# Kernel tuning notes

Hardware: AMD Instinct MI355X
Metric: run time of the kernel (lower is better)

## Reference

```python
import jax, jax.numpy as jnp
import numpy as np

BS, NUM_PATCH, N_VARS, PATCH_LEN, D_MODEL = 32, 64, 321, 12, 128
TIME_RATIO, FREQ_RATIO = 0.5, 0.4


def setup_inputs() -> dict:
    key = jax.random.key(0)
    ks = jax.random.split(key, 7)
    x = jax.random.normal(ks[0], (BS, NUM_PATCH, N_VARS, PATCH_LEN), jnp.float32)
    W_in = jax.random.normal(ks[1], (PATCH_LEN, D_MODEL), jnp.float32) / np.sqrt(PATCH_LEN)
    b_in = jnp.zeros((D_MODEL,), jnp.float32)
    W_out = jax.random.normal(ks[2], (D_MODEL, PATCH_LEN), jnp.float32) / np.sqrt(D_MODEL)
    b_out = jnp.zeros((PATCH_LEN,), jnp.float32)
    # nn.Parameter(torch.zeros(1,1,1)) in the original; use small random scalars so grads are non-trivial
    time_mask_token = jax.random.normal(ks[3], (), jnp.float32) * 0.02
    freq_mask_token = jax.random.normal(ks[4], (), jnp.float32) * 0.02
    return {"x": x, "W_in": W_in, "b_in": b_in, "W_out": W_out, "b_out": b_out,
            "time_mask_token": time_mask_token, "freq_mask_token": freq_mask_token}


def _scatter_mask(idx, num_patch):
    # idx: [bs, n_vars, k] patch indices to mask (set False). Returns bool [bs, num_patch, n_vars].
    bs, nv, k = idx.shape
    m = jnp.ones((bs, num_patch, nv), dtype=bool)
    b = jnp.arange(bs)[:, None, None]
    v = jnp.arange(nv)[None, :, None]
    return m.at[b, idx, v].set(False)


def reference(x, W_in, b_in, W_out, b_out, time_mask_token, freq_mask_token):
    bs, num_patch, n_vars, patch_len = x.shape

    # patch2emb applied per token (equivalent to the gather-encode path since the
    # projection is pointwise per patch): [bs, np, nv, d_model]
    emb = jnp.einsum('bpvl,ld->bpvd', x, W_in) + b_in

    # ---- time masking: mask patches with highest coefficient of variation ----
    cv = jnp.std(x, axis=-1, ddof=1) / (jnp.mean(x, axis=-1) + 1e-6)  # [bs, np, nv]
    k_t = int(num_patch * TIME_RATIO)
    _, idx_t = jax.lax.top_k(jnp.transpose(cv, (0, 2, 1)), k_t)       # [bs, nv, k_t]
    mask_t = _scatter_mask(idx_t, num_patch)                           # True = keep
    tokens_t = jnp.where(mask_t[..., None], emb, time_mask_token)
    out_t = jnp.einsum('bpvd,dl->bpvl', tokens_t, W_out) + b_out

    # ---- freq masking: mask patches with lowest mean FFT magnitude ----
    mag = jnp.abs(jnp.fft.rfft(x, axis=-1))                            # [bs, np, nv, pl//2+1]
    score = mag.mean(axis=-1)                                          # [bs, np, nv]
    k_f = int(num_patch * FREQ_RATIO)
    _, idx_f = jax.lax.top_k(-jnp.transpose(score, (0, 2, 1)), k_f)    # smallest scores
    mask_f = _scatter_mask(idx_f, num_patch)
    tokens_f = jnp.where(mask_f[..., None], emb, freq_mask_token)
    out_f = jnp.einsum('bpvd,dl->bpvl', tokens_f, W_out) + b_out

    return out_t * 0.5 + out_f * 0.5
```

## Files before the change

kernel.cpp:

```cpp
#include <hip/hip_runtime.h>
#include <math.h>

constexpr int BS = 32, NV = 321, PL = 12, DM = 128;
constexpr int KT = 32;
constexpr int KF = 25;
constexpr int VB = 8;
constexpr int NCHUNK = 41;
constexpr int SST = 72;

__device__ __forceinline__ unsigned ord(float f) {
  unsigned u = __float_as_uint(f);
  return ((int)u < 0) ? ~u : (u | 0x80000000u);
}

__global__ void prep_kernel(const float* __restrict__ W_in,
                            const float* __restrict__ b_in,
                            const float* __restrict__ W_out,
                            const float* __restrict__ b_out,
                            const float* __restrict__ tt,
                            const float* __restrict__ ft,
                            float* __restrict__ prep) {
  int t = threadIdx.x;
  if (t < 144) {
    int i = t / 12, l = t % 12;
    const float4* Wi = (const float4*)(W_in + i * DM);
    float s = 0.f;
#pragma unroll 8
    for (int d4 = 0; d4 < 32; ++d4) {
      float4 a = Wi[d4];
      const float* wo = W_out + d4 * 48 + l;
      s += a.x * wo[0] + a.y * wo[12] + a.z * wo[24] + a.w * wo[36];
    }
    prep[t] = s;
  } else if (t < 168) {
    int l = (t - 144) % 12;
    float cs = 0.f, cb = 0.f;
#pragma unroll 8
    for (int d = 0; d < DM; ++d) {
      float w = W_out[d * 12 + l];
      cs += w;
      cb += b_in[d] * w;
    }
    if (t < 156) {
      prep[144 + l] = cb;
      prep[156 + l] = tt[0] * cs;
    } else {
      prep[168 + l] = ft[0] * cs;
    }
  } else if (t < 180) {
    prep[180 + (t - 168)] = b_out[t - 168];
  }
}

__global__ __launch_bounds__(256) void fused_kernel(
    const float* __restrict__ x, const float* __restrict__ prep,
    float* __restrict__ out) {
  __shared__ float scv[VB * SST];
  __shared__ float sfs[VB * SST];
  __shared__ __align__(16) float spp[192];
  __shared__ unsigned long long smT[VB], smF[VB];

  const int t = threadIdx.x;
  const int chunk = blockIdx.x;
  const int b = blockIdx.y;
  const int v0 = chunk * VB;
  const bool full = (chunk < 40);
  const int nv = full ? VB : 1;

  const float* xb = x + ((size_t)(b * 64) * NV + v0) * PL;

  float xr[2][12];
  int pp[2], vvv[2];
  if (full) {
#pragma unroll
    for (int h = 0; h < 2; ++h) {
      const int j = t + 256 * h;
      const int p = j >> 3, vv = j & 7;
      pp[h] = p;
      vvv[h] = vv;
      const float4* src = (const float4*)(xb + ((size_t)p * NV + vv) * PL);
      float4 a = src[0], bb = src[1], c = src[2];
      xr[h][0] = a.x;  xr[h][1] = a.y;  xr[h][2] = a.z;  xr[h][3] = a.w;
      xr[h][4] = bb.x; xr[h][5] = bb.y; xr[h][6] = bb.z; xr[h][7] = bb.w;
      xr[h][8] = c.x;  xr[h][9] = c.y;  xr[h][10] = c.z; xr[h][11] = c.w;
    }
  } else {
    pp[0] = t & 63;
    vvv[0] = 0;
    pp[1] = 0;
    vvv[1] = 0;
    if (t < 64) {
      const float4* src = (const float4*)(xb + (size_t)t * NV * PL);
      float4 a = src[0], bb = src[1], c = src[2];
      xr[0][0] = a.x;  xr[0][1] = a.y;  xr[0][2] = a.z;  xr[0][3] = a.w;
      xr[0][4] = bb.x; xr[0][5] = bb.y; xr[0][6] = bb.z; xr[0][7] = bb.w;
      xr[0][8] = c.x;  xr[0][9] = c.y;  xr[0][10] = c.z; xr[0][11] = c.w;
    }
  }

  if (t < 192) spp[t] = prep[t];

  const float H = 0.86602540378443864676f;
#pragma unroll
  for (int h = 0; h < 2; ++h) {
    const bool valid = full || (h == 0 && t < 64);
    if (valid) {
      const float* xv = xr[h];
      float s = 0.f;
#pragma unroll
      for (int i = 0; i < 12; ++i) s += xv[i];
      const float m = s * (1.0f / 12.0f);
      float ss = 0.f;
#pragma unroll
      for (int i = 0; i < 12; ++i) {
        float d = xv[i] - m;
        ss += d * d;
      }
      const float cv = sqrtf(ss * (1.0f / 11.0f)) / (m + 1e-6f);

      const float e1 = xv[1] + xv[11], e2 = xv[2] + xv[10], e3 = xv[3] + xv[9],
                  e4 = xv[4] + xv[8], e5 = xv[5] + xv[7];
      const float o1 = xv[1] - xv[11], o2 = xv[2] - xv[10], o3 = xv[3] - xv[9],
                  o4 = xv[4] - xv[8], o5 = xv[5] - xv[7];
      float mag = fabsf(xv[0] + xv[6] + e1 + e2 + e3 + e4 + e5);
      float re = xv[0] - xv[6] + H * (e1 - e5) + 0.5f * (e2 - e4);
      float im = 0.5f * (o1 + o5) + H * (o2 + o4) + o3;
      mag += sqrtf(re * re + im * im);
      re = xv[0] + xv[6] + 0.5f * (e1 + e5) - 0.5f * (e2 + e4) - e3;
      im = H * (o1 + o2 - o4 - o5);
      mag += sqrtf(re * re + im * im);
      re = xv[0] - xv[6] - e2 + e4;
      im = o1 - o3 + o5;
      mag += sqrtf(re * re + im * im);
      re = xv[0] + xv[6] - 0.5f * (e1 + e2 + e4 + e5) + e3;
      im = H * (o1 - o2 + o4 - o5);
      mag += sqrtf(re * re + im * im);
      re = xv[0] - xv[6] + H * (e5 - e1) + 0.5f * (e2 - e4);
      im = 0.5f * (o1 + o5) - H * (o2 + o4) + o3;
      mag += sqrtf(re * re + im * im);
      re = xv[0] + xv[6] - e1 + e2 - e3 + e4 - e5;
      mag += fabsf(re);
      const float fs = mag * (1.0f / 7.0f);

      scv[vvv[h] * SST + pp[h]] = cv;
      sfs[vvv[h] * SST + pp[h]] = fs;
    }
  }
  __syncthreads();

  const int wv = t >> 6, lane = t & 63;
#pragma unroll
  for (int k = 0; k < 2; ++k) {
    const int vv = wv * 2 + k;
    if (vv < nv) {
      const unsigned ut = ord(scv[vv * SST + lane]);
      const unsigned uf = ~ord(sfs[vv * SST + lane]);
      unsigned tht = 0, thf = 0;
#pragma unroll
      for (int bit = 31; bit >= 0; --bit) {
        const unsigned ct = tht | (1u << bit);
        const unsigned cf = thf | (1u << bit);
        const unsigned long long bt = __ballot(ut >= ct);
        const unsigned long long bf = __ballot(uf >= cf);
        if (__popcll(bt) >= KT) tht = ct;
        if (__popcll(bf) >= KF) thf = cf;
      }
      const unsigned long long pre = (1ull << lane) - 1ull;
      const int gt_t = __popcll(__ballot(ut > tht));
      const int rt = __popcll(__ballot(ut == tht) & pre);
      const bool masked_t = (ut > tht) || ((ut == tht) && (rt < KT - gt_t));
      const int gt_f = __popcll(__ballot(uf > thf));
      const int rf = __popcll(__ballot(uf == thf) & pre);
      const bool masked_f = (uf > thf) || ((uf == thf) && (rf < KF - gt_f));
      const unsigned long long bkt = __ballot(!masked_t);
      const unsigned long long bkf = __ballot(!masked_f);
      if (lane == 0) {
        smT[vv] = bkt;
        smF[vv] = bkf;
      }
    }
  }
  __syncthreads();

  float E0[12], E1[12];
#pragma unroll
  for (int l = 0; l < 12; ++l) {
    E0[l] = spp[144 + l];
    E1[l] = spp[144 + l];
  }
  const float4* M4 = (const float4*)spp;
#pragma unroll
  for (int i = 0; i < 12; ++i) {
    float4 m0 = M4[i * 3], m1 = M4[i * 3 + 1], m2 = M4[i * 3 + 2];
    float a0 = xr[0][i], a1 = xr[1][i];
    E0[0] += a0 * m0.x;  E0[1] += a0 * m0.y;
    E0[2] += a0 * m0.z;  E0[3] += a0 * m0.w;
    E0[4] += a0 * m1.x;  E0[5] += a0 * m1.y;
    E0[6] += a0 * m1.z;  E0[7] += a0 * m1.w;
    E0[8] += a0 * m2.x;  E0[9] += a0 * m2.y;
    E0[10] += a0 * m2.z; E0[11] += a0 * m2.w;
    E1[0] += a1 * m0.x;  E1[1] += a1 * m0.y;
    E1[2] += a1 * m0.z;  E1[3] += a1 * m0.w;
    E1[4] += a1 * m1.x;  E1[5] += a1 * m1.y;
    E1[6] += a1 * m1.z;  E1[7] += a1 * m1.w;
    E1[8] += a1 * m2.x;  E1[9] += a1 * m2.y;
    E1[10] += a1 * m2.z; E1[11] += a1 * m2.w;
  }
#pragma unroll
  for (int h = 0; h < 2; ++h) {
    const bool valid = full || (h == 0 && t < 64);
    if (valid) {
      const int p = pp[h], vv = vvv[h];
      const bool kt = (smT[vv] >> p) & 1ull;
      const bool kf = (smF[vv] >> p) & 1ull;
      const float* E = (h == 0) ? E0 : E1;
      float o[12];
#pragma unroll
      for (int l = 0; l < 12; ++l) {
        float e = E[l];
        float at = kt ? e : spp[156 + l];
        float af = kf ? e : spp[168 + l];
        o[l] = 0.5f * (at + af) + spp[180 + l];
      }
      float* op = out + ((size_t)(b * 64 + p) * NV + v0 + vv) * PL;
      ((float4*)op)[0] = make_float4(o[0], o[1], o[2], o[3]);
      ((float4*)op)[1] = make_float4(o[4], o[5], o[6], o[7]);
      ((float4*)op)[2] = make_float4(o[8], o[9], o[10], o[11]);
    }
  }
}

extern "C" void kernel_launch(void* const* d_in, const int* in_sizes, int n_in,
                              void* d_out, int out_size, void* d_ws,
                              size_t ws_size, hipStream_t stream) {
  const float* x = (const float*)d_in[0];
  const float* W_in = (const float*)d_in[1];
  const float* b_in = (const float*)d_in[2];
  const float* W_out = (const float*)d_in[3];
  const float* b_out = (const float*)d_in[4];
  const float* tt = (const float*)d_in[5];
  const float* ft = (const float*)d_in[6];
  float* out = (float*)d_out;
  float* prep = (float*)d_ws;

  hipLaunchKernelGGL(prep_kernel, dim3(1), dim3(192), 0, stream, W_in, b_in,
                     W_out, b_out, tt, ft, prep);
  hipLaunchKernelGGL(fused_kernel, dim3(NCHUNK, BS), dim3(256), 0, stream, x,
                     prep, out);
}
```

Measured before the change: 117.7 us.

## Split fused kernel into score/mask kernel and flat per-token decode kernel

Replaces the single fused kernel with two passes. A score kernel (512 threads, one token per thread) computes CV and FFT scores and the per-variable top-k masks, writes them to workspace, and also folds in the weight-prep work through an extra block column. A flat decode kernel then rereads x with fully contiguous indexing and applies the folded 12x12 projection and the masks. This trades a second full read of x plus a mask round trip through global memory for better coalescing and occupancy. It also removes the separate prep launch, but the prep stored in the score launch has no ordering guarantee against the other score blocks. The prep index mapping was also changed from i=t/12, l=t%12 to l=t/12, i=t%12, which the decode kernel matches by reading ws[l*12+i].

Result: faster. 110.0 us (-6.5%).

```diff
diff --git a/kernel.cpp b/kernel.cpp
--- a/kernel.cpp
+++ b/kernel.cpp
@@ -7,227 +7,205 @@
 constexpr int VB = 8;
 constexpr int NCHUNK = 41;
 constexpr int SST = 72;
+constexpr int TOTPV = BS * 64 * NV;
+constexpr int MASK_BYTE_OFF = 4096;
 
 __device__ __forceinline__ unsigned ord(float f) {
   unsigned u = __float_as_uint(f);
   return ((int)u < 0) ? ~u : (u | 0x80000000u);
 }
 
-__global__ void prep_kernel(const float* __restrict__ W_in,
-                            const float* __restrict__ b_in,
-                            const float* __restrict__ W_out,
-                            const float* __restrict__ b_out,
-                            const float* __restrict__ tt,
-                            const float* __restrict__ ft,
-                            float* __restrict__ prep) {
-  int t = threadIdx.x;
-  if (t < 144) {
-    int i = t / 12, l = t % 12;
-    const float4* Wi = (const float4*)(W_in + i * DM);
-    float s = 0.f;
-#pragma unroll 8
-    for (int d4 = 0; d4 < 32; ++d4) {
-      float4 a = Wi[d4];
-      const float* wo = W_out + d4 * 48 + l;
-      s += a.x * wo[0] + a.y * wo[12] + a.z * wo[24] + a.w * wo[36];
-    }
-    prep[t] = s;
-  } else if (t < 168) {
-    int l = (t - 144) % 12;
-    float cs = 0.f, cb = 0.f;
-#pragma unroll 8
-    for (int d = 0; d < DM; ++d) {
-      float w = W_out[d * 12 + l];
-      cs += w;
-      cb += b_in[d] * w;
-    }
-    if (t < 156) {
-      prep[144 + l] = cb;
-      prep[156 + l] = tt[0] * cs;
-    } else {
-      prep[168 + l] = ft[0] * cs;
-    }
-  } else if (t < 180) {
-    prep[180 + (t - 168)] = b_out[t - 168];
-  }
-}
-
-__global__ __launch_bounds__(256) void fused_kernel(
-    const float* __restrict__ x, const float* __restrict__ prep,
-    float* __restrict__ out) {
-  __shared__ float scv[VB * SST];
-  __shared__ float sfs[VB * SST];
-  __shared__ __align__(16) float spp[192];
-  __shared__ unsigned long long smT[VB], smF[VB];
-
+__global__ __launch_bounds__(512, 8) void score_kernel(
+    const float* __restrict__ x, const float* __restrict__ W_in,
+    const float* __restrict__ b_in, const float* __restrict__ W_out,
+    const float* __restrict__ b_out, const float* __restrict__ tt,
+    const float* __restrict__ ft, float* __restrict__ ws) {
   const int t = threadIdx.x;
   const int chunk = blockIdx.x;
   const int b = blockIdx.y;
+
+  if (chunk == NCHUNK) {
+    if (b != 0) return;
+    if (t < 144) {
+      const int l = t / 12, i = t % 12;
+      const float4* Wi = (const float4*)(W_in + i * DM);
+      float s = 0.f;
+#pragma unroll 8
+      for (int d4 = 0; d4 < 32; ++d4) {
+        float4 a = Wi[d4];
+        const float* wo = W_out + d4 * 48 + l;
+        s += a.x * wo[0] + a.y * wo[12] + a.z * wo[24] + a.w * wo[36];
+      }
+      ws[t] = s;
+    } else if (t < 168) {
+      const int l = (t - 144) % 12;
+      float cs = 0.f, cb = 0.f;
+#pragma unroll 8
+      for (int d = 0; d < DM; ++d) {
+        float w = W_out[d * 12 + l];
+        cs += w;
+        cb += b_in[d] * w;
+      }
+      if (t < 156) {
+        ws[144 + l] = cb;
+        ws[156 + l] = tt[0] * cs;
+      } else {
+        ws[168 + l] = ft[0] * cs;
+      }
+    } else if (t < 180) {
+      ws[180 + (t - 168)] = b_out[t - 168];
+    }
+    return;
+  }
+
+  __shared__ float scv[VB * SST];
+  __shared__ float sfs[VB * SST];
+
   const int v0 = chunk * VB;
   const bool full = (chunk < 40);
   const int nv = full ? VB : 1;
 
   const float* xb = x + ((size_t)(b * 64) * NV + v0) * PL;
 
-  float xr[2][12];
-  int pp[2], vvv[2];
+  int p, vv;
+  bool valid;
   if (full) {
-#pragma unroll
-    for (int h = 0; h < 2; ++h) {
-      const int j = t + 256 * h;
-      const int p = j >> 3, vv = j & 7;
-      pp[h] = p;
-      vvv[h] = vv;
-      const float4* src = (const float4*)(xb + ((size_t)p * NV + vv) * PL);
-      float4 a = src[0], bb = src[1], c = src[2];
-      xr[h][0] = a.x;  xr[h][1] = a.y;  xr[h][2] = a.z;  xr[h][3] = a.w;
-      xr[h][4] = bb.x; xr[h][5] = bb.y; xr[h][6] = bb.z; xr[h][7] = bb.w;
-      xr[h][8] = c.x;  xr[h][9] = c.y;  xr[h][10] = c.z; xr[h][11] = c.w;
-    }
+    p = t >> 3;
+    vv = t & 7;
+    valid = true;
   } else {
-    pp[0] = t & 63;
-    vvv[0] = 0;
-    pp[1] = 0;
-    vvv[1] = 0;
-    if (t < 64) {
-      const float4* src = (const float4*)(xb + (size_t)t * NV * PL);
-      float4 a = src[0], bb = src[1], c = src[2];
-      xr[0][0] = a.x;  xr[0][1] = a.y;  xr[0][2] = a.z;  xr[0][3] = a.w;
-      xr[0][4] = bb.x; xr[0][5] = bb.y; xr[0][6] = bb.z; xr[0][7] = bb.w;
-      xr[0][8] = c.x;  xr[0][9] = c.y;  xr[0][10] = c.z; xr[0][11] = c.w;
-    }
-  }
-
-  if (t < 192) spp[t] = prep[t];
-
-  const float H = 0.86602540378443864676f;
-#pragma unroll
-  for (int h = 0; h < 2; ++h) {
-    const bool valid = full || (h == 0 && t < 64);
-    if (valid) {
-      const float* xv = xr[h];
-      float s = 0.f;
-#pragma unroll
-      for (int i = 0; i < 12; ++i) s += xv[i];
-      const float m = s * (1.0f / 12.0f);
-      float ss = 0.f;
-#pragma unroll
-      for (int i = 0; i < 12; ++i) {
-        float d = xv[i] - m;
-        ss += d * d;
-      }
-      const float cv = sqrtf(ss * (1.0f / 11.0f)) / (m + 1e-6f);
-
-      const float e1 = xv[1] + xv[11], e2 = xv[2] + xv[10], e3 = xv[3] + xv[9],
-                  e4 = xv[4] + xv[8], e5 = xv[5] + xv[7];
-      const float o1 = xv[1] - xv[11], o2 = xv[2] - xv[10], o3 = xv[3] - xv[9],
-                  o4 = xv[4] - xv[8], o5 = xv[5] - xv[7];
-      float mag = fabsf(xv[0] + xv[6] + e1 + e2 + e3 + e4 + e5);
-      float re = xv[0] - xv[6] + H * (e1 - e5) + 0.5f * (e2 - e4);
-      float im = 0.5f * (o1 + o5) + H * (o2 + o4) + o3;
-      mag += sqrtf(re * re + im * im);
-      re = xv[0] + xv[6] + 0.5f * (e1 + e5) - 0.5f * (e2 + e4) - e3;
-      im = H * (o1 + o2 - o4 - o5);
-      mag += sqrtf(re * re + im * im);
-      re = xv[0] - xv[6] - e2 + e4;
-      im = o1 - o3 + o5;
-      mag += sqrtf(re * re + im * im);
-      re = xv[0] + xv[6] - 0.5f * (e1 + e2 + e4 + e5) + e3;
-      im = H * (o1 - o2 + o4 - o5);
-      mag += sqrtf(re * re + im * im);
-      re = xv[0] - xv[6] + H * (e5 - e1) + 0.5f * (e2 - e4);
-      im = 0.5f * (o1 + o5) - H * (o2 + o4) + o3;
-      mag += sqrtf(re * re + im * im);
-      re = xv[0] + xv[6] - e1 + e2 - e3 + e4 - e5;
-      mag += fabsf(re);
-      const float fs = mag * (1.0f / 7.0f);
-
-      scv[vvv[h] * SST + pp[h]] = cv;
-      sfs[vvv[h] * SST + pp[h]] = fs;
-    }
+    p = t & 63;
+    vv = 0;
+    valid = (t < 64);
+  }
+
+  if (valid) {
+    const float4* src = (const float4*)(xb + ((size_t)p * NV + vv) * PL);
+    float4 a = src[0], bb = src[1], c = src[2];
+    float xv[12];
+    xv[0] = a.x;  xv[1] = a.y;  xv[2] = a.z;  xv[3] = a.w;
+    xv[4] = bb.x; xv[5] = bb.y; xv[6] = bb.z; xv[7] = bb.w;
+    xv[8] = c.x;  xv[9] = c.y;  xv[10] = c.z; xv[11] = c.w;
+
+    float s = 0.f;
+#pragma unroll
+    for (int i = 0; i < 12; ++i) s += xv[i];
+    const float m = s * (1.0f / 12.0f);
+    float ss = 0.f;
+#pragma unroll
+    for (int i = 0; i < 12; ++i) {
+      float d = xv[i] - m;
+      ss += d * d;
+    }
+    const float cv = sqrtf(ss * (1.0f / 11.0f)) / (m + 1e-6f);
+
+    const float H = 0.86602540378443864676f;
+    const float e1 = xv[1] + xv[11], e2 = xv[2] + xv[10], e3 = xv[3] + xv[9],
+                e4 = xv[4] + xv[8], e5 = xv[5] + xv[7];
+    const float o1 = xv[1] - xv[11], o2 = xv[2] - xv[10], o3 = xv[3] - xv[9],
+                o4 = xv[4] - xv[8], o5 = xv[5] - xv[7];
+    float mag = fabsf(xv[0] + xv[6] + e1 + e2 + e3 + e4 + e5);
+    float re = xv[0] - xv[6] + H * (e1 - e5) + 0.5f * (e2 - e4);
+    float im = 0.5f * (o1 + o5) + H * (o2 + o4) + o3;
+    mag += sqrtf(re * re + im * im);
+    re = xv[0] + xv[6] + 0.5f * (e1 + e5) - 0.5f * (e2 + e4) - e3;
+    im = H * (o1 + o2 - o4 - o5);
+    mag += sqrtf(re * re + im * im);
+    re = xv[0] - xv[6] - e2 + e4;
+    im = o1 - o3 + o5;
+    mag += sqrtf(re * re + im * im);
+    re = xv[0] + xv[6] - 0.5f * (e1 + e2 + e4 + e5) + e3;
+    im = H * (o1 - o2 + o4 - o5);
+    mag += sqrtf(re * re + im * im);
+    re = xv[0] - xv[6] + H * (e5 - e1) + 0.5f * (e2 - e4);
+    im = 0.5f * (o1 + o5) - H * (o2 + o4) + o3;
+    mag += sqrtf(re * re + im * im);
+    re = xv[0] + xv[6] - e1 + e2 - e3 + e4 - e5;
+    mag += fabsf(re);
+    const float fs = mag * (1.0f / 7.0f);
+
+    scv[vv * SST + p] = cv;
+    sfs[vv * SST + p] = fs;
   }
   __syncthreads();
 
   const int wv = t >> 6, lane = t & 63;
-#pragma unroll
-  for (int k = 0; k < 2; ++k) {
-    const int vv = wv * 2 + k;
-    if (vv < nv) {
-      const unsigned ut = ord(scv[vv * SST + lane]);
-      const unsigned uf = ~ord(sfs[vv * SST + lane]);
-      unsigned tht = 0, thf = 0;
-#pragma unroll
-      for (int bit = 31; bit >= 0; --bit) {
-        const unsigned ct = tht | (1u << bit);
-        const unsigned cf = thf | (1u << bit);
-        const unsigned long long bt = __ballot(ut >= ct);
-        const unsigned long long bf = __ballot(uf >= cf);
-        if (__popcll(bt) >= KT) tht = ct;
-        if (__popcll(bf) >= KF) thf = cf;
-      }
-      const unsigned long long pre = (1ull << lane) - 1ull;
-      const int gt_t = __popcll(__ballot(ut > tht));
-      const int rt = __popcll(__ballot(ut == tht) & pre);
-      const bool masked_t = (ut > tht) || ((ut == tht) && (rt < KT - gt_t));
-      const int gt_f = __popcll(__ballot(uf > thf));
-      const int rf = __popcll(__ballot(uf == thf) & pre);
-      const bool masked_f = (uf > thf) || ((uf == thf) && (rf < KF - gt_f));
-      const unsigned long long bkt = __ballot(!masked_t);
-      const unsigned long long bkf = __ballot(!masked_f);
-      if (lane == 0) {
-        smT[vv] = bkt;
-        smF[vv] = bkf;
-      }
-    }
-  }
-  __syncthreads();
-
-  float E0[12], E1[12];
-#pragma unroll
-  for (int l = 0; l < 12; ++l) {
-    E0[l] = spp[144 + l];
-    E1[l] = spp[144 + l];
-  }
-  const float4* M4 = (const float4*)spp;
-#pragma unroll
-  for (int i = 0; i < 12; ++i) {
-    float4 m0 = M4[i * 3], m1 = M4[i * 3 + 1], m2 = M4[i * 3 + 2];
-    float a0 = xr[0][i], a1 = xr[1][i];
-    E0[0] += a0 * m0.x;  E0[1] += a0 * m0.y;
-    E0[2] += a0 * m0.z;  E0[3] += a0 * m0.w;
-    E0[4] += a0 * m1.x;  E0[5] += a0 * m1.y;
-    E0[6] += a0 * m1.z;  E0[7] += a0 * m1.w;
-    E0[8] += a0 * m2.x;  E0[9] += a0 * m2.y;
-    E0[10] += a0 * m2.z; E0[11] += a0 * m2.w;
-    E1[0] += a1 * m0.x;  E1[1] += a1 * m0.y;
-    E1[2] += a1 * m0.z;  E1[3] += a1 * m0.w;
-    E1[4] += a1 * m1.x;  E1[5] += a1 * m1.y;
-    E1[6] += a1 * m1.z;  E1[7] += a1 * m1.w;
-    E1[8] += a1 * m2.x;  E1[9] += a1 * m2.y;
-    E1[10] += a1 * m2.z; E1[11] += a1 * m2.w;
-  }
-#pragma unroll
-  for (int h = 0; h < 2; ++h) {
-    const bool valid = full || (h == 0 && t < 64);
-    if (valid) {
-      const int p = pp[h], vv = vvv[h];
-      const bool kt = (smT[vv] >> p) & 1ull;
-      const bool kf = (smF[vv] >> p) & 1ull;
-      const float* E = (h == 0) ? E0 : E1;
-      float o[12];
-#pragma unroll
-      for (int l = 0; l < 12; ++l) {
-        float e = E[l];
-        float at = kt ? e : spp[156 + l];
-        float af = kf ? e : spp[168 + l];
-        o[l] = 0.5f * (at + af) + spp[180 + l];
-      }
-      float* op = out + ((size_t)(b * 64 + p) * NV + v0 + vv) * PL;
-      ((float4*)op)[0] = make_float4(o[0], o[1], o[2], o[3]);
-      ((float4*)op)[1] = make_float4(o[4], o[5], o[6], o[7]);
-      ((float4*)op)[2] = make_float4(o[8], o[9], o[10], o[11]);
-    }
-  }
+  if (wv < nv) {
+    const unsigned ut = ord(scv[wv * SST + lane]);
+    const unsigned uf = ~ord(sfs[wv * SST + lane]);
+    unsigned tht = 0, thf = 0;
+#pragma unroll
+    for (int bit = 31; bit >= 0; --bit) {
+      const unsigned ct = tht | (1u << bit);
+      const unsigned cf = thf | (1u << bit);
+      const unsigned long long bt = __ballot(ut >= ct);
+      const unsigned long long bf = __ballot(uf >= cf);
+      if (__popcll(bt) >= KT) tht = ct;
+      if (__popcll(bf) >= KF) thf = cf;
+    }
+    const unsigned long long pre = (1ull << lane) - 1ull;
+    const int gt_t = __popcll(__ballot(ut > tht));
+    const int rt = __popcll(__ballot(ut == tht) & pre);
+    const bool masked_t = (ut > tht) || ((ut == tht) && (rt < KT - gt_t));
+    const int gt_f = __popcll(__ballot(uf > thf));
+    const int rf = __popcll(__ballot(uf == thf) & pre);
+    const bool masked_f = (uf > thf) || ((uf == thf) && (rf < KF - gt_f));
+    const unsigned long long bkt = __ballot(!masked_t);
+    const unsigned long long bkf = __ballot(!masked_f);
+    if (lane == 0) {
+      unsigned long long* mk =
+          (unsigned long long*)((char*)ws + MASK_BYTE_OFF);
+      const int vidx = b * NV + v0 + wv;
+      mk[2 * vidx] = bkt;
+      mk[2 * vidx + 1] = bkf;
+    }
+  }
+}
+
+__global__ __launch_bounds__(256, 8) void decode_kernel(
+    const float* __restrict__ x, const float* __restrict__ ws,
+    float* __restrict__ out) {
+  const int g = blockIdx.x * 256 + threadIdx.x;
+  const unsigned v = (unsigned)g % NV;
+  const unsigned bp = (unsigned)g / NV;
+  const int p = bp & 63;
+  const int b = bp >> 6;
+
+  const float4* src = (const float4*)(x + (size_t)g * PL);
+  float4 a = src[0], bb = src[1], c = src[2];
+  float xv[12];
+  xv[0] = a.x;  xv[1] = a.y;  xv[2] = a.z;  xv[3] = a.w;
+  xv[4] = bb.x; xv[5] = bb.y; xv[6] = bb.z; xv[7] = bb.w;
+  xv[8] = c.x;  xv[9] = c.y;  xv[10] = c.z; xv[11] = c.w;
+
+  const unsigned long long* mk =
+      (const unsigned long long*)((const char*)ws + MASK_BYTE_OFF);
+  const int vidx = b * NV + (int)v;
+  const unsigned long long mT = mk[2 * vidx];
+  const unsigned long long mF = mk[2 * vidx + 1];
+  const bool kt = (mT >> p) & 1ull;
+  const bool kf = (mF >> p) & 1ull;
+
+  float o[12];
+#pragma unroll
+  for (int l0 = 0; l0 < 12; l0 += 4) {
+#pragma unroll
+    for (int l = l0; l < l0 + 4; ++l) {
+      const float* Ml = ws + l * 12;
+      float e = ws[144 + l];
+#pragma unroll
+      for (int i = 0; i < 12; ++i) e = fmaf(xv[i], Ml[i], e);
+      const float at = kt ? e : ws[156 + l];
+      const float af = kf ? e : ws[168 + l];
+      o[l] = 0.5f * (at + af) + ws[180 + l];
+    }
+    if (l0 < 8) __builtin_amdgcn_sched_barrier(0);
+  }
+
+  float* op = out + (size_t)g * PL;
+  ((float4*)op)[0] = make_float4(o[0], o[1], o[2], o[3]);
+  ((float4*)op)[1] = make_float4(o[4], o[5], o[6], o[7]);
+  ((float4*)op)[2] = make_float4(o[8], o[9], o[10], o[11]);
 }
 
 extern "C" void kernel_launch(void* const* d_in, const int* in_sizes, int n_in,
@@ -241,10 +219,10 @@
   const float* tt = (const float*)d_in[5];
   const float* ft = (const float*)d_in[6];
   float* out = (float*)d_out;
-  float* prep = (float*)d_ws;
-
-  hipLaunchKernelGGL(prep_kernel, dim3(1), dim3(192), 0, stream, W_in, b_in,
-                     W_out, b_out, tt, ft, prep);
-  hipLaunchKernelGGL(fused_kernel, dim3(NCHUNK, BS), dim3(256), 0, stream, x,
-                     prep, out);
-}
+  float* ws = (float*)d_ws;
+
+  hipLaunchKernelGGL(score_kernel, dim3(NCHUNK + 1, BS), dim3(512), 0, stream,
+                     x, W_in, b_in, W_out, b_out, tt, ft, ws);
+  hipLaunchKernelGGL(decode_kernel, dim3(TOTPV / 256), dim3(256), 0, stream, x,
+                     ws, out);
+}
```
